# Performance work log

Measured on AMD Instinct MI355X. Metric: run time of the kernel, lower is better.

## Reference

```python
import jax, jax.numpy as jnp
import numpy as np

N = 50000        # nodes
E = 1_600_000    # edges
F_IN = 128       # input feature dim
EMB = 48         # emb_size
HID = 48         # hidden_size
OUT = 64         # out_sizes[0]
K = 7            # Chebyshev order


def setup_inputs() -> dict:
    key = jax.random.key(0)
    ks = jax.random.split(key, 8)
    x = jax.random.normal(ks[0], (N, F_IN), dtype=jnp.float32)
    edge_index = jax.random.randint(ks[1], (2, E), 0, N, dtype=jnp.int32)
    edge_weight = jax.random.uniform(ks[2], (E,), dtype=jnp.float32)
    W_in = jax.random.normal(ks[3], (F_IN, EMB), jnp.float32) / np.float32(np.sqrt(F_IN))
    b_in = jnp.zeros((EMB,), jnp.float32)
    W_cheb = jax.random.normal(ks[4], (K, EMB, HID), jnp.float32) / np.float32(np.sqrt(EMB))
    b_cheb = jnp.zeros((HID,), jnp.float32)
    W_out = jax.random.normal(ks[5], (HID, OUT), jnp.float32) / np.float32(np.sqrt(HID))
    b_out = jnp.zeros((OUT,), jnp.float32)
    return dict(x=x, edge_index=edge_index, edge_weight=edge_weight,
                W_in=W_in, b_in=b_in, W_cheb=W_cheb, b_cheb=b_cheb,
                W_out=W_out, b_out=b_out)


def reference(x, edge_index, edge_weight, W_in, b_in, W_cheb, b_cheb, W_out, b_out):
    row, col = edge_index[0], edge_index[1]
    # PyG ChebConv sym normalization with lambda_max=2:
    #   L_hat = 2/lambda_max * (I - D^-1/2 A D^-1/2) - I = -D^-1/2 A D^-1/2
    deg = jax.ops.segment_sum(edge_weight, row, num_segments=N)
    dinv = jnp.where(deg > 0, jax.lax.rsqrt(deg), 0.0)
    norm = -dinv[row] * edge_weight * dinv[col]  # [E]

    # input Linear + ReLU (Dropout is identity at eval)
    xf = jax.nn.relu(x @ W_in + b_in)  # [N, EMB]

    def prop(t):
        # out[i] = sum_{(j->i) in E} norm_e * t[j]
        return jax.ops.segment_sum(norm[:, None] * t[row], col, num_segments=N)

    # Chebyshev recursion: T0 = x, T1 = L_hat x, T_k = 2 L_hat T_{k-1} - T_{k-2}
    Tx0 = xf
    out = Tx0 @ W_cheb[0]
    Tx1 = prop(Tx0)
    out = out + Tx1 @ W_cheb[1]
    for k in range(2, K):
        Tx2 = 2.0 * prop(Tx1) - Tx0
        out = out + Tx2 @ W_cheb[k]
        Tx0, Tx1 = Tx1, Tx2
    out = out + b_cheb

    y = jax.nn.relu(out)          # ReLU after ChebConv (out_drop = identity at eval)
    y = y @ W_out + b_out          # output Linear
    return (y, xf)
```

## Files before the change

kernel.cpp:

```cpp
#include <hip/hip_runtime.h>
#include <hip/hip_fp16.h>

#define N_NODES 50000
#define N_EDGES 1600000
#define F_IN    128
#define EMB     48
#define HID     48
#define OUTF    64
#define KCH     7
#define TPAD    64

#define NR    8
#define RANGE (N_NODES / NR)
#define BPR   64
#define SLICE (N_EDGES / BPR)
#define HTHREADS 512
#define NBLK  ((N_NODES + 255) / 256)
#define NTILES (N_NODES / 16)

typedef __attribute__((ext_vector_type(8))) _Float16 half8;
typedef __attribute__((ext_vector_type(4))) float f32x4;

#define PROP_GATHER_LOOP(TSRC)                                                  \
    {                                                                           \
        int e16 = s + ((e - s) & ~15);                                          \
        for (; p < e16; p += 16) {                                              \
            float ww[16]; uint2 hv[16];                                         \
            _Pragma("unroll")                                                   \
            for (int j = 0; j < 16; ++j) {                                      \
                uint2 er = edges[p + j];                                        \
                ww[j] = __uint_as_float(er.y);                                  \
                hv[j] = *reinterpret_cast<const uint2*>(                        \
                    TSRC + (size_t)er.x * TPAD + 4 * lane);                     \
            }                                                                   \
            _Pragma("unroll")                                                   \
            for (int j = 0; j < 16; ++j) {                                      \
                __half2 h01 = *reinterpret_cast<__half2*>(&hv[j].x);            \
                __half2 h23 = *reinterpret_cast<__half2*>(&hv[j].y);            \
                a0 += ww[j] * __low2float(h01);                                 \
                a1 += ww[j] * __high2float(h01);                                \
                a2 += ww[j] * __low2float(h23);                                 \
                a3 += ww[j] * __high2float(h23);                                \
            }                                                                   \
        }                                                                       \
        int e4b = p + ((e - p) & ~3);                                           \
        for (; p < e4b; p += 4) {                                               \
            float ww[4]; uint2 hv[4];                                           \
            _Pragma("unroll")                                                   \
            for (int j = 0; j < 4; ++j) {                                       \
                uint2 er = edges[p + j];                                        \
                ww[j] = __uint_as_float(er.y);                                  \
                hv[j] = *reinterpret_cast<const uint2*>(                        \
                    TSRC + (size_t)er.x * TPAD + 4 * lane);                     \
            }                                                                   \
            _Pragma("unroll")                                                   \
            for (int j = 0; j < 4; ++j) {                                       \
                __half2 h01 = *reinterpret_cast<__half2*>(&hv[j].x);            \
                __half2 h23 = *reinterpret_cast<__half2*>(&hv[j].y);            \
                a0 += ww[j] * __low2float(h01);                                 \
                a1 += ww[j] * __high2float(h01);                                \
                a2 += ww[j] * __low2float(h23);                                 \
                a3 += ww[j] * __high2float(h23);                                \
            }                                                                   \
        }                                                                       \
        for (; p < e; ++p) {                                                    \
            uint2 er = edges[p];                                                \
            float wv = __uint_as_float(er.y);                                   \
            uint2 hv = *reinterpret_cast<const uint2*>(                         \
                TSRC + (size_t)er.x * TPAD + 4 * lane);                         \
            __half2 h01 = *reinterpret_cast<__half2*>(&hv.x);                   \
            __half2 h23 = *reinterpret_cast<__half2*>(&hv.y);                   \
            a0 += wv * __low2float(h01);                                        \
            a1 += wv * __high2float(h01);                                       \
            a2 += wv * __low2float(h23);                                        \
            a3 += wv * __high2float(h23);                                       \
        }                                                                       \
    }

__global__ __launch_bounds__(HTHREADS) void hist_part_kernel(
    const int* __restrict__ row, const int* __restrict__ col,
    const float* __restrict__ w,
    unsigned short* __restrict__ pc, float* __restrict__ pd,
    unsigned short* __restrict__ rank16)
{
    __shared__ unsigned lc32[RANGE / 2];
    __shared__ float    ld[RANGE];
    int t = threadIdx.x;
    for (int i = t; i < RANGE / 2; i += HTHREADS) lc32[i] = 0u;
    for (int i = t; i < RANGE; i += HTHREADS) ld[i] = 0.f;
    __syncthreads();
    int r = blockIdx.x / BPR;
    int b = blockIdx.x % BPR;
    int base = r * RANGE;
    int lo = b * SLICE;
    for (int e0 = lo + t * 4; e0 < lo + SLICE; e0 += HTHREADS * 4) {
        int4   c4 = *(const int4*)&col[e0];
        int4   r4 = *(const int4*)&row[e0];
        float4 w4 = *(const float4*)&w[e0];
        #pragma unroll
        for (int j = 0; j < 4; ++j) {
            int c  = (j == 0) ? c4.x : (j == 1) ? c4.y : (j == 2) ? c4.z : c4.w;
            int rw = (j == 0) ? r4.x : (j == 1) ? r4.y : (j == 2) ? r4.z : r4.w;
            float we = (j == 0) ? w4.x : (j == 1) ? w4.y : (j == 2) ? w4.z : w4.w;
            int ci = c - base;
            if ((unsigned)ci < RANGE) {
                unsigned sh = (ci & 1) * 16;
                unsigned old = atomicAdd(&lc32[ci >> 1], 1u << sh);
                rank16[e0 + j] = (unsigned short)((old >> sh) & 0xFFFFu);
            }
            int ri = rw - base;
            if ((unsigned)ri < RANGE) atomicAdd(&ld[ri], we);
        }
    }
    __syncthreads();
    unsigned short* pcb = pc + (size_t)blockIdx.x * RANGE;
    float*          pdb = pd + (size_t)blockIdx.x * RANGE;
    for (int i = t; i < RANGE; i += HTHREADS) {
        pcb[i] = (unsigned short)((lc32[i >> 1] >> ((i & 1) * 16)) & 0xFFFFu);
        pdb[i] = ld[i];
    }
}

__global__ __launch_bounds__(256) void reduce_kernel(
    unsigned short* __restrict__ pc, const float* __restrict__ pd,
    float* __restrict__ dinv, int* __restrict__ off, int* __restrict__ bsum)
{
    int t = threadIdx.x;
    int n = blockIdx.x * 256 + t;
    int c = 0; float d = 0.f;
    if (n < N_NODES) {
        int r = n / RANGE, i = n - r * RANGE;
        size_t base = (size_t)r * BPR * RANGE + i;
        unsigned csum = 0;
        for (int b = 0; b < BPR; ++b) {
            size_t idx = base + (size_t)b * RANGE;
            unsigned x = pc[idx];
            pc[idx] = (unsigned short)csum;
            csum += x;
            d += pd[idx];
        }
        c = (int)csum;
        dinv[n] = d > 0.f ? rsqrtf(d) : 0.f;
    }
    int lane = t & 63, wid = t >> 6;
    int v = c;
    for (int s = 1; s < 64; s <<= 1) {
        int u = __shfl_up(v, s);
        if (lane >= s) v += u;
    }
    __shared__ int ws[4];
    if (lane == 63) ws[wid] = v;
    __syncthreads();
    int wb = 0;
    for (int i = 0; i < 4; ++i) if (i < wid) wb += ws[i];
    int ex = (v - c) + wb;
    if (n < N_NODES) off[n] = ex;
    if (t == 255) bsum[blockIdx.x] = ex + c;
}

__global__ __launch_bounds__(256) void bsum_scan_kernel(
    int* __restrict__ bsum, int* __restrict__ off)
{
    int t = threadIdx.x;
    int orig = (t < NBLK) ? bsum[t] : 0;
    int lane = t & 63, wid = t >> 6;
    int v = orig;
    for (int s = 1; s < 64; s <<= 1) {
        int u = __shfl_up(v, s);
        if (lane >= s) v += u;
    }
    __shared__ int ws[4];
    if (lane == 63) ws[wid] = v;
    __syncthreads();
    int wb = 0;
    for (int i = 0; i < 4; ++i) if (i < wid) wb += ws[i];
    int ex = (v - orig) + wb;
    if (t < NBLK) bsum[t] = ex;
    if (t == NBLK - 1) off[N_NODES] = ex + orig;
}

__global__ __launch_bounds__(256) void add_off_kernel(
    int* __restrict__ off, const int* __restrict__ bsum)
{
    int n = blockIdx.x * 256 + threadIdx.x;
    if (n < N_NODES) off[n] += bsum[n >> 8];
}

__global__ __launch_bounds__(256) void scatter_flat_kernel(
    const int* __restrict__ row, const int* __restrict__ col,
    const float* __restrict__ w, const float* __restrict__ dinv,
    const int* __restrict__ off, const unsigned short* __restrict__ pc,
    const unsigned short* __restrict__ rank16, uint2* __restrict__ edges)
{
    int tid = blockIdx.x * 256 + threadIdx.x;
    int e0 = tid * 4;
    if (e0 >= N_EDGES) return;
    int b = e0 / SLICE;
    int4   c4 = *(const int4*)&col[e0];
    int4   r4 = *(const int4*)&row[e0];
    float4 w4 = *(const float4*)&w[e0];
    ushort4 k4 = *(const ushort4*)&rank16[e0];
    #pragma unroll
    for (int j = 0; j < 4; ++j) {
        int c  = (j == 0) ? c4.x : (j == 1) ? c4.y : (j == 2) ? c4.z : c4.w;
        int rw = (j == 0) ? r4.x : (j == 1) ? r4.y : (j == 2) ? r4.z : r4.w;
        float we = (j == 0) ? w4.x : (j == 1) ? w4.y : (j == 2) ? w4.z : w4.w;
        int rk = (j == 0) ? k4.x : (j == 1) ? k4.y : (j == 2) ? k4.z : k4.w;
        int rg = c / RANGE;
        int clocal = c - rg * RANGE;
        int pre = pc[(size_t)(rg * BPR + b) * RANGE + clocal];
        float nr = -dinv[rw] * we * dinv[c];
        int pos = off[c] + pre + rk;
        edges[pos] = make_uint2((unsigned)rw, __float_as_uint(nr));
    }
}

__global__ __launch_bounds__(256) void xf_mfma_kernel(
    const float* __restrict__ x, const float* __restrict__ Win,
    const float* __restrict__ bin, float* __restrict__ xf_out,
    __half* __restrict__ T0h)
{
    __shared__ half8 Wf[3][4][64];
    __shared__ float bs[EMB];
    int t = threadIdx.x;
    for (int idx = t; idx < 3 * 4 * 64; idx += 256) {
        int j = idx >> 8;
        int rem = idx & 255;
        int s = rem >> 6;
        int l = rem & 63;
        int colw = j * 16 + (l & 15);
        int k0 = s * 32 + (l >> 4) * 8;
        half8 v;
        #pragma unroll
        for (int i = 0; i < 8; ++i)
            v[i] = (_Float16)Win[(k0 + i) * EMB + colw];
        Wf[j][s][l] = v;
    }
    if (t < EMB) bs[t] = bin[t];
    __syncthreads();

    int wid = t >> 6, lane = t & 63;
    int nt = blockIdx.x * 4 + wid;
    if (nt >= NTILES) return;
    int n0 = nt * 16;
    int arow = lane & 15, kg = lane >> 4;

    const float* xr = x + (size_t)(n0 + arow) * F_IN + kg * 8;
    half8 a[4];
    #pragma unroll
    for (int s = 0; s < 4; ++s) {
        f32x4 lo = *reinterpret_cast<const f32x4*>(xr + s * 32);
        f32x4 hi = *reinterpret_cast<const f32x4*>(xr + s * 32 + 4);
        half8 av;
        av[0] = (_Float16)lo[0]; av[1] = (_Float16)lo[1];
        av[2] = (_Float16)lo[2]; av[3] = (_Float16)lo[3];
        av[4] = (_Float16)hi[0]; av[5] = (_Float16)hi[1];
        av[6] = (_Float16)hi[2]; av[7] = (_Float16)hi[3];
        a[s] = av;
    }

    f32x4 c0 = {0.f, 0.f, 0.f, 0.f}, c1 = c0, c2 = c0;
    #pragma unroll
    for (int s = 0; s < 4; ++s) {
        c0 = __builtin_amdgcn_mfma_f32_16x16x32_f16(a[s], Wf[0][s][lane], c0, 0, 0, 0);
        c1 = __builtin_amdgcn_mfma_f32_16x16x32_f16(a[s], Wf[1][s][lane], c1, 0, 0, 0);
        c2 = __builtin_amdgcn_mfma_f32_16x16x32_f16(a[s], Wf[2][s][lane], c2, 0, 0, 0);
    }

    int ccol = lane & 15;
    #pragma unroll
    for (int j = 0; j < 3; ++j) {
        int colg = j * 16 + ccol;
        float bias = bs[colg];
        f32x4 cj = (j == 0) ? c0 : (j == 1) ? c1 : c2;
        #pragma unroll
        for (int r = 0; r < 4; ++r) {
            int n = n0 + kg * 4 + r;
            float v = fmaxf(cj[r] + bias, 0.f);
            xf_out[(size_t)n * EMB + colg] = v;
            T0h[(size_t)n * TPAD + colg] = __float2half_rn(v);
        }
    }
    {
        int n = n0 + (lane >> 2);
        int cp = 48 + (lane & 3) * 4;
        *reinterpret_cast<uint2*>(T0h + (size_t)n * TPAD + cp) = make_uint2(0u, 0u);
    }
}

__global__ __launch_bounds__(256) void prop_k1_kernel(
    const int* __restrict__ off, const uint2* __restrict__ edges,
    const __half* __restrict__ T0, __half* __restrict__ T1,
    const float* __restrict__ W0, const float* __restrict__ W1,
    float* __restrict__ out_acc)
{
    __shared__ float W0s[EMB * HID];
    __shared__ float W1s[EMB * HID];
    __shared__ float tdS[16][EMB + 1];
    __shared__ float t0S[16][EMB + 1];
    int t = threadIdx.x;
    for (int i = t; i < EMB * HID; i += 256) { W0s[i] = W0[i]; W1s[i] = W1[i]; }
    __syncthreads();

    int grp = t >> 4, lane = t & 15;
    int g = blockIdx.x * 16 + grp;

    float a0 = 0.f, a1 = 0.f, a2 = 0.f, a3 = 0.f;
    if (lane < 12) {
        int s = off[g], e = off[g + 1];
        int p = s;
        PROP_GATHER_LOOP(T0)
        uint2 tv = *reinterpret_cast<const uint2*>(T0 + (size_t)g * TPAD + 4 * lane);
        __half2 t01 = *reinterpret_cast<__half2*>(&tv.x);
        __half2 t23 = *reinterpret_cast<__half2*>(&tv.y);
        t0S[grp][4 * lane]     = __low2float(t01);
        t0S[grp][4 * lane + 1] = __high2float(t01);
        t0S[grp][4 * lane + 2] = __low2float(t23);
        t0S[grp][4 * lane + 3] = __high2float(t23);
        tdS[grp][4 * lane]     = a0;
        tdS[grp][4 * lane + 1] = a1;
        tdS[grp][4 * lane + 2] = a2;
        tdS[grp][4 * lane + 3] = a3;
    }
    {
        __half2 h01, h23;
        h01.x = __float2half_rn(a0); h01.y = __float2half_rn(a1);
        h23.x = __float2half_rn(a2); h23.y = __float2half_rn(a3);
        uint2 ov;
        ov.x = *reinterpret_cast<unsigned*>(&h01);
        ov.y = *reinterpret_cast<unsigned*>(&h23);
        *reinterpret_cast<uint2*>(T1 + (size_t)g * TPAD + 4 * lane) = ov;
    }

    float o0 = 0.f, o1 = 0.f, o2 = 0.f;
#pragma unroll 8
    for (int c = 0; c < EMB; ++c) {
        float t1v = tdS[grp][c];
        float t0v = t0S[grp][c];
        o0 += t1v * W1s[c * HID + lane]      + t0v * W0s[c * HID + lane];
        o1 += t1v * W1s[c * HID + lane + 16] + t0v * W0s[c * HID + lane + 16];
        o2 += t1v * W1s[c * HID + lane + 32] + t0v * W0s[c * HID + lane + 32];
    }
    float* orow = out_acc + (size_t)g * HID;
    orow[lane]      = o0;
    orow[lane + 16] = o1;
    orow[lane + 32] = o2;
}

__global__ __launch_bounds__(256) void prop_fused_kernel(
    const int* __restrict__ off, const uint2* __restrict__ edges,
    const __half* __restrict__ tsrc, const __half* __restrict__ tprev,
    __half* __restrict__ tdst, const float* __restrict__ Wk,
    float* __restrict__ out_acc)
{
    __shared__ float Ws[EMB * HID];
    __shared__ float tdS[16][EMB + 1];
    int t = threadIdx.x;
    for (int i = t; i < EMB * HID; i += 256) Ws[i] = Wk[i];
    __syncthreads();

    int grp = t >> 4, lane = t & 15;
    int g = blockIdx.x * 16 + grp;

    float a0 = 0.f, a1 = 0.f, a2 = 0.f, a3 = 0.f;
    if (lane < 12) {
        int s = off[g], e = off[g + 1];
        int p = s;
        PROP_GATHER_LOOP(tsrc)
        uint2 tv = *reinterpret_cast<const uint2*>(tprev + (size_t)g * TPAD + 4 * lane);
        __half2 t01 = *reinterpret_cast<__half2*>(&tv.x);
        __half2 t23 = *reinterpret_cast<__half2*>(&tv.y);
        a0 = 2.f * a0 - __low2float(t01);
        a1 = 2.f * a1 - __high2float(t01);
        a2 = 2.f * a2 - __low2float(t23);
        a3 = 2.f * a3 - __high2float(t23);
        tdS[grp][4 * lane]     = a0;
        tdS[grp][4 * lane + 1] = a1;
        tdS[grp][4 * lane + 2] = a2;
        tdS[grp][4 * lane + 3] = a3;
    }
    {
        __half2 h01, h23;
        h01.x = __float2half_rn(a0); h01.y = __float2half_rn(a1);
        h23.x = __float2half_rn(a2); h23.y = __float2half_rn(a3);
        uint2 ov;
        ov.x = *reinterpret_cast<unsigned*>(&h01);
        ov.y = *reinterpret_cast<unsigned*>(&h23);
        *reinterpret_cast<uint2*>(tdst + (size_t)g * TPAD + 4 * lane) = ov;
    }

    float o0 = 0.f, o1 = 0.f, o2 = 0.f;
#pragma unroll 8
    for (int c = 0; c < EMB; ++c) {
        float tv = tdS[grp][c];
        o0 += tv * Ws[c * HID + lane];
        o1 += tv * Ws[c * HID + lane + 16];
        o2 += tv * Ws[c * HID + lane + 32];
    }
    float* orow = out_acc + (size_t)g * HID;
    orow[lane]      += o0;
    orow[lane + 16] += o1;
    orow[lane + 32] += o2;
}

__global__ __launch_bounds__(256) void prop_final_kernel(
    const int* __restrict__ off, const uint2* __restrict__ edges,
    const __half* __restrict__ tsrc, const __half* __restrict__ tprev,
    const float* __restrict__ Wk, const float* __restrict__ out_acc,
    const float* __restrict__ bch, const float* __restrict__ Wout,
    const float* __restrict__ bout, float* __restrict__ y)
{
    __shared__ float Ws[EMB * HID];
    __shared__ float Wo[HID * OUTF];
    __shared__ float tdS[16][EMB + 1];
    __shared__ float vS[16][HID + 1];
    __shared__ float bchS[HID];
    __shared__ float boS[OUTF];
    int t = threadIdx.x;
    for (int i = t; i < EMB * HID; i += 256) Ws[i] = Wk[i];
    for (int i = t; i < HID * OUTF; i += 256) Wo[i] = Wout[i];
    if (t < HID) bchS[t] = bch[t];
    if (t < OUTF) boS[t] = bout[t];
    __syncthreads();

    int grp = t >> 4, lane = t & 15;
    int g = blockIdx.x * 16 + grp;

    float a0 = 0.f, a1 = 0.f, a2 = 0.f, a3 = 0.f;
    if (lane < 12) {
        int s = off[g], e = off[g + 1];
        int p = s;
        PROP_GATHER_LOOP(tsrc)
        uint2 tv = *reinterpret_cast<const uint2*>(tprev + (size_t)g * TPAD + 4 * lane);
        __half2 t01 = *reinterpret_cast<__half2*>(&tv.x);
        __half2 t23 = *reinterpret_cast<__half2*>(&tv.y);
        a0 = 2.f * a0 - __low2float(t01);
        a1 = 2.f * a1 - __high2float(t01);
        a2 = 2.f * a2 - __low2float(t23);
        a3 = 2.f * a3 - __high2float(t23);
        tdS[grp][4 * lane]     = a0;
        tdS[grp][4 * lane + 1] = a1;
        tdS[grp][4 * lane + 2] = a2;
        tdS[grp][4 * lane + 3] = a3;
    }

    float o0 = 0.f, o1 = 0.f, o2 = 0.f;
#pragma unroll 8
    for (int c = 0; c < EMB; ++c) {
        float tv = tdS[grp][c];
        o0 += tv * Ws[c * HID + lane];
        o1 += tv * Ws[c * HID + lane + 16];
        o2 += tv * Ws[c * HID + lane + 32];
    }
    const float* orow = out_acc + (size_t)g * HID;
    vS[grp][lane]      = fmaxf(orow[lane]      + o0 + bchS[lane],      0.f);
    vS[grp][lane + 16] = fmaxf(orow[lane + 16] + o1 + bchS[lane + 16], 0.f);
    vS[grp][lane + 32] = fmaxf(orow[lane + 32] + o2 + bchS[lane + 32], 0.f);

    float y0 = boS[4 * lane], y1 = boS[4 * lane + 1];
    float y2 = boS[4 * lane + 2], y3 = boS[4 * lane + 3];
#pragma unroll 8
    for (int h = 0; h < HID; ++h) {
        float v = vS[grp][h];
        float4 w4 = *reinterpret_cast<const float4*>(&Wo[h * OUTF + 4 * lane]);
        y0 += v * w4.x; y1 += v * w4.y; y2 += v * w4.z; y3 += v * w4.w;
    }
    *reinterpret_cast<float4*>(y + (size_t)g * OUTF + 4 * lane) =
        make_float4(y0, y1, y2, y3);
}

extern "C" void kernel_launch(void* const* d_in, const int* in_sizes, int n_in,
                              void* d_out, int out_size, void* d_ws, size_t ws_size,
                              hipStream_t stream)
{
    const float* x    = (const float*)d_in[0];
    const int*   ei   = (const int*)d_in[1];
    const float* ew   = (const float*)d_in[2];
    const float* Win  = (const float*)d_in[3];
    const float* bin  = (const float*)d_in[4];
    const float* Wch  = (const float*)d_in[5];
    const float* bch  = (const float*)d_in[6];
    const float* Wout = (const float*)d_in[7];
    const float* bout = (const float*)d_in[8];

    const int* row = ei;
    const int* col = ei + N_EDGES;

    float* y_out  = (float*)d_out;
    float* xf_out = (float*)d_out + (size_t)N_NODES * OUTF;

    char* p = (char*)d_ws;
    auto carve = [&](size_t bytes) {
        void* q = p;
        p += (bytes + 255) & ~(size_t)255;
        return q;
    };
    unsigned short* pc = (unsigned short*)carve((size_t)NR * BPR * RANGE * 2);
    float*    pd  = (float*)carve((size_t)NR * BPR * RANGE * 4);
    unsigned short* rank16 = (unsigned short*)carve((size_t)N_EDGES * 2);
    float*    dinv = (float*)carve(N_NODES * 4);
    int*      off  = (int*)  carve((N_NODES + 1) * 4);
    int*      bsum = (int*)  carve(NBLK * 4);
    uint2*    edges = (uint2*)carve((size_t)N_EDGES * 8);
    float*    out_acc = (float*)carve((size_t)N_NODES * HID * 4);
    __half*   T0h = (__half*)carve((size_t)N_NODES * TPAD * 2);
    __half*   TAh = (__half*)carve((size_t)N_NODES * TPAD * 2);
    __half*   TBh = (__half*)carve((size_t)N_NODES * TPAD * 2);
    __half*   TCh = (__half*)carve((size_t)N_NODES * TPAD * 2);

    hist_part_kernel<<<NR * BPR, HTHREADS, 0, stream>>>(row, col, ew, pc, pd, rank16);
    reduce_kernel<<<NBLK, 256, 0, stream>>>(pc, pd, dinv, off, bsum);
    bsum_scan_kernel<<<1, 256, 0, stream>>>(bsum, off);
    add_off_kernel<<<NBLK, 256, 0, stream>>>(off, bsum);
    scatter_flat_kernel<<<(N_EDGES / 4 + 255) / 256, 256, 0, stream>>>(
        row, col, ew, dinv, off, pc, rank16, edges);

    xf_mfma_kernel<<<(NTILES + 3) / 4, 256, 0, stream>>>(x, Win, bin, xf_out, T0h);

    const int prop_grid = NTILES;

    prop_k1_kernel<<<prop_grid, 256, 0, stream>>>(off, edges, T0h, TAh,
                                                  Wch, Wch + EMB * HID, out_acc);
    const __half* A = T0h;
    __half*       B = TAh;
    __half* bufs[3] = {TBh, TCh, TAh};
    for (int k = 2; k < KCH - 1; ++k) {
        __half* C = bufs[(k - 2) % 3];
        prop_fused_kernel<<<prop_grid, 256, 0, stream>>>(off, edges, B, A,
                                                         C, Wch + (size_t)k * EMB * HID, out_acc);
        A = B; B = C;
    }
    prop_final_kernel<<<prop_grid, 256, 0, stream>>>(off, edges, B, A,
                                                     Wch + (size_t)(KCH - 1) * EMB * HID,
                                                     out_acc, bch, Wout, bout, y_out);
}
```

Measured before the change: 340.4 us.

## Defer Chebyshev weight GEMMs to a single MFMA epilogue over stored Tx buffers

The per-step dense GEMMs (Tx_k @ W_cheb[k]) and the out_acc read-modify-write are removed from the propagation kernels, so each prop step becomes a pure sparse gather writing fp16 Tx_k into one contiguous 7-slice buffer. A new epilogue kernel then computes the concatenated [T0..T6] @ W_cheb with fp16 MFMA, adds bias and ReLU, and applies the output Linear also with MFMA. The intent is to lighten the latency-bound gather kernels, drop their shared-memory weight loads and fp32 accumulator traffic, and use matrix cores for the dense work. In exchange the epilogue must re-read all seven fp16 Tx buffers, and the intermediate activations plus W_out are rounded to fp16, which lowers precision.

Result: faster. 327.5 us (-3.8%).

```diff
diff --git a/kernel.cpp b/kernel.cpp
--- a/kernel.cpp
+++ b/kernel.cpp
@@ -9,6 +9,7 @@
 #define OUTF    64
 #define KCH     7
 #define TPAD    64
+#define KSL     14
 
 #define NR    8
 #define RANGE (N_NODES / NR)
@@ -288,77 +289,12 @@
     }
 }
 
-__global__ __launch_bounds__(256) void prop_k1_kernel(
-    const int* __restrict__ off, const uint2* __restrict__ edges,
-    const __half* __restrict__ T0, __half* __restrict__ T1,
-    const float* __restrict__ W0, const float* __restrict__ W1,
-    float* __restrict__ out_acc)
-{
-    __shared__ float W0s[EMB * HID];
-    __shared__ float W1s[EMB * HID];
-    __shared__ float tdS[16][EMB + 1];
-    __shared__ float t0S[16][EMB + 1];
-    int t = threadIdx.x;
-    for (int i = t; i < EMB * HID; i += 256) { W0s[i] = W0[i]; W1s[i] = W1[i]; }
-    __syncthreads();
-
-    int grp = t >> 4, lane = t & 15;
-    int g = blockIdx.x * 16 + grp;
-
-    float a0 = 0.f, a1 = 0.f, a2 = 0.f, a3 = 0.f;
-    if (lane < 12) {
-        int s = off[g], e = off[g + 1];
-        int p = s;
-        PROP_GATHER_LOOP(T0)
-        uint2 tv = *reinterpret_cast<const uint2*>(T0 + (size_t)g * TPAD + 4 * lane);
-        __half2 t01 = *reinterpret_cast<__half2*>(&tv.x);
-        __half2 t23 = *reinterpret_cast<__half2*>(&tv.y);
-        t0S[grp][4 * lane]     = __low2float(t01);
-        t0S[grp][4 * lane + 1] = __high2float(t01);
-        t0S[grp][4 * lane + 2] = __low2float(t23);
-        t0S[grp][4 * lane + 3] = __high2float(t23);
-        tdS[grp][4 * lane]     = a0;
-        tdS[grp][4 * lane + 1] = a1;
-        tdS[grp][4 * lane + 2] = a2;
-        tdS[grp][4 * lane + 3] = a3;
-    }
-    {
-        __half2 h01, h23;
-        h01.x = __float2half_rn(a0); h01.y = __float2half_rn(a1);
-        h23.x = __float2half_rn(a2); h23.y = __float2half_rn(a3);
-        uint2 ov;
-        ov.x = *reinterpret_cast<unsigned*>(&h01);
-        ov.y = *reinterpret_cast<unsigned*>(&h23);
-        *reinterpret_cast<uint2*>(T1 + (size_t)g * TPAD + 4 * lane) = ov;
-    }
-
-    float o0 = 0.f, o1 = 0.f, o2 = 0.f;
-#pragma unroll 8
-    for (int c = 0; c < EMB; ++c) {
-        float t1v = tdS[grp][c];
-        float t0v = t0S[grp][c];
-        o0 += t1v * W1s[c * HID + lane]      + t0v * W0s[c * HID + lane];
-        o1 += t1v * W1s[c * HID + lane + 16] + t0v * W0s[c * HID + lane + 16];
-        o2 += t1v * W1s[c * HID + lane + 32] + t0v * W0s[c * HID + lane + 32];
-    }
-    float* orow = out_acc + (size_t)g * HID;
-    orow[lane]      = o0;
-    orow[lane + 16] = o1;
-    orow[lane + 32] = o2;
-}
-
-__global__ __launch_bounds__(256) void prop_fused_kernel(
+__global__ __launch_bounds__(256) void prop_pure_kernel(
     const int* __restrict__ off, const uint2* __restrict__ edges,
     const __half* __restrict__ tsrc, const __half* __restrict__ tprev,
-    __half* __restrict__ tdst, const float* __restrict__ Wk,
-    float* __restrict__ out_acc)
-{
-    __shared__ float Ws[EMB * HID];
-    __shared__ float tdS[16][EMB + 1];
-    int t = threadIdx.x;
-    for (int i = t; i < EMB * HID; i += 256) Ws[i] = Wk[i];
-    __syncthreads();
-
+    __half* __restrict__ tdst, int cheb_mode)
+{
+    int t = threadIdx.x;
     int grp = t >> 4, lane = t & 15;
     int g = blockIdx.x * 16 + grp;
 
@@ -367,106 +303,127 @@
         int s = off[g], e = off[g + 1];
         int p = s;
         PROP_GATHER_LOOP(tsrc)
-        uint2 tv = *reinterpret_cast<const uint2*>(tprev + (size_t)g * TPAD + 4 * lane);
-        __half2 t01 = *reinterpret_cast<__half2*>(&tv.x);
-        __half2 t23 = *reinterpret_cast<__half2*>(&tv.y);
-        a0 = 2.f * a0 - __low2float(t01);
-        a1 = 2.f * a1 - __high2float(t01);
-        a2 = 2.f * a2 - __low2float(t23);
-        a3 = 2.f * a3 - __high2float(t23);
-        tdS[grp][4 * lane]     = a0;
-        tdS[grp][4 * lane + 1] = a1;
-        tdS[grp][4 * lane + 2] = a2;
-        tdS[grp][4 * lane + 3] = a3;
-    }
-    {
-        __half2 h01, h23;
-        h01.x = __float2half_rn(a0); h01.y = __float2half_rn(a1);
-        h23.x = __float2half_rn(a2); h23.y = __float2half_rn(a3);
-        uint2 ov;
-        ov.x = *reinterpret_cast<unsigned*>(&h01);
-        ov.y = *reinterpret_cast<unsigned*>(&h23);
-        *reinterpret_cast<uint2*>(tdst + (size_t)g * TPAD + 4 * lane) = ov;
-    }
-
-    float o0 = 0.f, o1 = 0.f, o2 = 0.f;
-#pragma unroll 8
-    for (int c = 0; c < EMB; ++c) {
-        float tv = tdS[grp][c];
-        o0 += tv * Ws[c * HID + lane];
-        o1 += tv * Ws[c * HID + lane + 16];
-        o2 += tv * Ws[c * HID + lane + 32];
-    }
-    float* orow = out_acc + (size_t)g * HID;
-    orow[lane]      += o0;
-    orow[lane + 16] += o1;
-    orow[lane + 32] += o2;
-}
-
-__global__ __launch_bounds__(256) void prop_final_kernel(
-    const int* __restrict__ off, const uint2* __restrict__ edges,
-    const __half* __restrict__ tsrc, const __half* __restrict__ tprev,
-    const float* __restrict__ Wk, const float* __restrict__ out_acc,
-    const float* __restrict__ bch, const float* __restrict__ Wout,
-    const float* __restrict__ bout, float* __restrict__ y)
-{
-    __shared__ float Ws[EMB * HID];
-    __shared__ float Wo[HID * OUTF];
-    __shared__ float tdS[16][EMB + 1];
-    __shared__ float vS[16][HID + 1];
+        if (cheb_mode) {
+            uint2 tv = *reinterpret_cast<const uint2*>(tprev + (size_t)g * TPAD + 4 * lane);
+            __half2 t01 = *reinterpret_cast<__half2*>(&tv.x);
+            __half2 t23 = *reinterpret_cast<__half2*>(&tv.y);
+            a0 = 2.f * a0 - __low2float(t01);
+            a1 = 2.f * a1 - __high2float(t01);
+            a2 = 2.f * a2 - __low2float(t23);
+            a3 = 2.f * a3 - __high2float(t23);
+        }
+    }
+    __half2 h01, h23;
+    h01.x = __float2half_rn(a0); h01.y = __float2half_rn(a1);
+    h23.x = __float2half_rn(a2); h23.y = __float2half_rn(a3);
+    uint2 ov;
+    ov.x = *reinterpret_cast<unsigned*>(&h01);
+    ov.y = *reinterpret_cast<unsigned*>(&h23);
+    *reinterpret_cast<uint2*>(tdst + (size_t)g * TPAD + 4 * lane) = ov;
+}
+
+__global__ __launch_bounds__(256) void cheb_epi_kernel(
+    const __half* __restrict__ Tall,
+    const float* __restrict__ Wch,
+    const float* __restrict__ bch,
+    const float* __restrict__ Wout,
+    const float* __restrict__ bout,
+    float* __restrict__ y)
+{
+    __shared__ half8 Wf[3][KSL][64];
+    __shared__ half8 Wo[4][2][64];
+    __shared__ _Float16 vSh[4][16][64];
     __shared__ float bchS[HID];
     __shared__ float boS[OUTF];
     int t = threadIdx.x;
-    for (int i = t; i < EMB * HID; i += 256) Ws[i] = Wk[i];
-    for (int i = t; i < HID * OUTF; i += 256) Wo[i] = Wout[i];
+    for (int idx = t; idx < 3 * KSL * 64; idx += 256) {
+        int j = idx / (KSL * 64);
+        int rem = idx - j * (KSL * 64);
+        int s = rem >> 6;
+        int l = rem & 63;
+        int colw = j * 16 + (l & 15);
+        int kch = s >> 1;
+        int kbase = (s & 1) * 32 + (l >> 4) * 8;
+        half8 v;
+        #pragma unroll
+        for (int i = 0; i < 8; ++i) {
+            int kloc = kbase + i;
+            v[i] = (kloc < EMB)
+                 ? (_Float16)Wch[(size_t)kch * EMB * HID + kloc * HID + colw]
+                 : (_Float16)0.f;
+        }
+        Wf[j][s][l] = v;
+    }
+    for (int idx = t; idx < 4 * 2 * 64; idx += 256) {
+        int jo = idx >> 7;
+        int rem = idx & 127;
+        int so = rem >> 6;
+        int l = rem & 63;
+        int colw = jo * 16 + (l & 15);
+        int kbase = so * 32 + (l >> 4) * 8;
+        half8 v;
+        #pragma unroll
+        for (int i = 0; i < 8; ++i) {
+            int kloc = kbase + i;
+            v[i] = (kloc < HID) ? (_Float16)Wout[kloc * OUTF + colw] : (_Float16)0.f;
+        }
+        Wo[jo][so][l] = v;
+    }
     if (t < HID) bchS[t] = bch[t];
     if (t < OUTF) boS[t] = bout[t];
     __syncthreads();
 
-    int grp = t >> 4, lane = t & 15;
-    int g = blockIdx.x * 16 + grp;
-
-    float a0 = 0.f, a1 = 0.f, a2 = 0.f, a3 = 0.f;
-    if (lane < 12) {
-        int s = off[g], e = off[g + 1];
-        int p = s;
-        PROP_GATHER_LOOP(tsrc)
-        uint2 tv = *reinterpret_cast<const uint2*>(tprev + (size_t)g * TPAD + 4 * lane);
-        __half2 t01 = *reinterpret_cast<__half2*>(&tv.x);
-        __half2 t23 = *reinterpret_cast<__half2*>(&tv.y);
-        a0 = 2.f * a0 - __low2float(t01);
-        a1 = 2.f * a1 - __high2float(t01);
-        a2 = 2.f * a2 - __low2float(t23);
-        a3 = 2.f * a3 - __high2float(t23);
-        tdS[grp][4 * lane]     = a0;
-        tdS[grp][4 * lane + 1] = a1;
-        tdS[grp][4 * lane + 2] = a2;
-        tdS[grp][4 * lane + 3] = a3;
-    }
-
-    float o0 = 0.f, o1 = 0.f, o2 = 0.f;
-#pragma unroll 8
-    for (int c = 0; c < EMB; ++c) {
-        float tv = tdS[grp][c];
-        o0 += tv * Ws[c * HID + lane];
-        o1 += tv * Ws[c * HID + lane + 16];
-        o2 += tv * Ws[c * HID + lane + 32];
-    }
-    const float* orow = out_acc + (size_t)g * HID;
-    vS[grp][lane]      = fmaxf(orow[lane]      + o0 + bchS[lane],      0.f);
-    vS[grp][lane + 16] = fmaxf(orow[lane + 16] + o1 + bchS[lane + 16], 0.f);
-    vS[grp][lane + 32] = fmaxf(orow[lane + 32] + o2 + bchS[lane + 32], 0.f);
-
-    float y0 = boS[4 * lane], y1 = boS[4 * lane + 1];
-    float y2 = boS[4 * lane + 2], y3 = boS[4 * lane + 3];
-#pragma unroll 8
-    for (int h = 0; h < HID; ++h) {
-        float v = vS[grp][h];
-        float4 w4 = *reinterpret_cast<const float4*>(&Wo[h * OUTF + 4 * lane]);
-        y0 += v * w4.x; y1 += v * w4.y; y2 += v * w4.z; y3 += v * w4.w;
-    }
-    *reinterpret_cast<float4*>(y + (size_t)g * OUTF + 4 * lane) =
-        make_float4(y0, y1, y2, y3);
+    int wid = t >> 6, lane = t & 63;
+    int nt = blockIdx.x * 4 + wid;
+    if (nt >= NTILES) return;
+    int n0 = nt * 16;
+    int arow = lane & 15, kg = lane >> 4;
+    int ccol = lane & 15;
+
+    f32x4 c0 = {0.f, 0.f, 0.f, 0.f}, c1 = c0, c2 = c0;
+    #pragma unroll
+    for (int s = 0; s < KSL; ++s) {
+        const __half* tp = Tall + (size_t)(s >> 1) * N_NODES * TPAD
+                         + (size_t)(n0 + arow) * TPAD + (s & 1) * 32 + kg * 8;
+        half8 af = *reinterpret_cast<const half8*>(tp);
+        c0 = __builtin_amdgcn_mfma_f32_16x16x32_f16(af, Wf[0][s][lane], c0, 0, 0, 0);
+        c1 = __builtin_amdgcn_mfma_f32_16x16x32_f16(af, Wf[1][s][lane], c1, 0, 0, 0);
+        c2 = __builtin_amdgcn_mfma_f32_16x16x32_f16(af, Wf[2][s][lane], c2, 0, 0, 0);
+    }
+    #pragma unroll
+    for (int j = 0; j < 3; ++j) {
+        int colg = j * 16 + ccol;
+        float bias = bchS[colg];
+        f32x4 cj = (j == 0) ? c0 : (j == 1) ? c1 : c2;
+        #pragma unroll
+        for (int r = 0; r < 4; ++r)
+            vSh[wid][kg * 4 + r][colg] = (_Float16)fmaxf(cj[r] + bias, 0.f);
+    }
+    {
+        int rr = lane >> 2;
+        int cp = 48 + (lane & 3) * 4;
+        *reinterpret_cast<uint2*>(&vSh[wid][rr][cp]) = make_uint2(0u, 0u);
+    }
+    __builtin_amdgcn_wave_barrier();
+
+    f32x4 y0 = {0.f, 0.f, 0.f, 0.f}, y1 = y0, y2 = y0, y3 = y0;
+    #pragma unroll
+    for (int so = 0; so < 2; ++so) {
+        half8 af = *reinterpret_cast<const half8*>(&vSh[wid][arow][so * 32 + kg * 8]);
+        y0 = __builtin_amdgcn_mfma_f32_16x16x32_f16(af, Wo[0][so][lane], y0, 0, 0, 0);
+        y1 = __builtin_amdgcn_mfma_f32_16x16x32_f16(af, Wo[1][so][lane], y1, 0, 0, 0);
+        y2 = __builtin_amdgcn_mfma_f32_16x16x32_f16(af, Wo[2][so][lane], y2, 0, 0, 0);
+        y3 = __builtin_amdgcn_mfma_f32_16x16x32_f16(af, Wo[3][so][lane], y3, 0, 0, 0);
+    }
+    #pragma unroll
+    for (int jo = 0; jo < 4; ++jo) {
+        int colg = jo * 16 + ccol;
+        float bias = boS[colg];
+        f32x4 cj = (jo == 0) ? y0 : (jo == 1) ? y1 : (jo == 2) ? y2 : y3;
+        #pragma unroll
+        for (int r = 0; r < 4; ++r)
+            y[(size_t)(n0 + kg * 4 + r) * OUTF + colg] = cj[r] + bias;
+    }
 }
 
 extern "C" void kernel_launch(void* const* d_in, const int* in_sizes, int n_in,
@@ -502,11 +459,7 @@
     int*      off  = (int*)  carve((N_NODES + 1) * 4);
     int*      bsum = (int*)  carve(NBLK * 4);
     uint2*    edges = (uint2*)carve((size_t)N_EDGES * 8);
-    float*    out_acc = (float*)carve((size_t)N_NODES * HID * 4);
-    __half*   T0h = (__half*)carve((size_t)N_NODES * TPAD * 2);
-    __half*   TAh = (__half*)carve((size_t)N_NODES * TPAD * 2);
-    __half*   TBh = (__half*)carve((size_t)N_NODES * TPAD * 2);
-    __half*   TCh = (__half*)carve((size_t)N_NODES * TPAD * 2);
+    __half*   Tall = (__half*)carve((size_t)KCH * N_NODES * TPAD * 2);
 
     hist_part_kernel<<<NR * BPR, HTHREADS, 0, stream>>>(row, col, ew, pc, pd, rank16);
     reduce_kernel<<<NBLK, 256, 0, stream>>>(pc, pd, dinv, off, bsum);
@@ -515,22 +468,18 @@
     scatter_flat_kernel<<<(N_EDGES / 4 + 255) / 256, 256, 0, stream>>>(
         row, col, ew, dinv, off, pc, rank16, edges);
 
-    xf_mfma_kernel<<<(NTILES + 3) / 4, 256, 0, stream>>>(x, Win, bin, xf_out, T0h);
+    const size_t TSTR = (size_t)N_NODES * TPAD;
+    xf_mfma_kernel<<<(NTILES + 3) / 4, 256, 0, stream>>>(x, Win, bin, xf_out, Tall);
 
     const int prop_grid = NTILES;
 
-    prop_k1_kernel<<<prop_grid, 256, 0, stream>>>(off, edges, T0h, TAh,
-                                                  Wch, Wch + EMB * HID, out_acc);
-    const __half* A = T0h;
-    __half*       B = TAh;
-    __half* bufs[3] = {TBh, TCh, TAh};
-    for (int k = 2; k < KCH - 1; ++k) {
-        __half* C = bufs[(k - 2) % 3];
-        prop_fused_kernel<<<prop_grid, 256, 0, stream>>>(off, edges, B, A,
-                                                         C, Wch + (size_t)k * EMB * HID, out_acc);
-        A = B; B = C;
-    }
-    prop_final_kernel<<<prop_grid, 256, 0, stream>>>(off, edges, B, A,
-                                                     Wch + (size_t)(KCH - 1) * EMB * HID,
-                                                     out_acc, bch, Wout, bout, y_out);
-}
+    prop_pure_kernel<<<prop_grid, 256, 0, stream>>>(off, edges, Tall, nullptr,
+                                                    Tall + TSTR, 0);
+    for (int k = 2; k < KCH; ++k) {
+        prop_pure_kernel<<<prop_grid, 256, 0, stream>>>(
+            off, edges, Tall + (size_t)(k - 1) * TSTR, Tall + (size_t)(k - 2) * TSTR,
+            Tall + (size_t)k * TSTR, 1);
+    }
+
+    cheb_epi_kernel<<<(NTILES + 3) / 4, 256, 0, stream>>>(Tall, Wch, bch, Wout, bout, y_out);
+}
```
